# Optimization experiments

Hardware: AMD Instinct MI355X
Metric: run time of the kernel (lower is better)

The kernel has to match this reference:

```python
import jax, jax.numpy as jnp
import numpy as np

DIM = 256      # in_channels == hidden_channels
INNER = 256    # heads * dim_head
HEADS = 4
DH = 64        # dim_head = hidden_channels // num_heads
EDGE_DIM = 512 # 2 * in_channels
FF = 1024      # 4 * dim ff expansion
DEPTH = 2
OUT = 1
N = 50000      # two stacked graphs of 25000 nodes
E = 100000
HALF = 25000


def setup_inputs() -> dict:
    key = jax.random.key(0)
    ks = iter(jax.random.split(key, 32))

    def lin(fan_in, fan_out):
        w = jax.random.normal(next(ks), (DEPTH, fan_in, fan_out), jnp.float32) * (1.0 / np.sqrt(fan_in))
        b = jnp.zeros((DEPTH, fan_out), jnp.float32)
        return w, b

    x = jax.random.normal(next(ks), (N, DIM), jnp.float32)
    edge_index = jax.random.randint(next(ks), (2, E), 0, HALF, dtype=jnp.int32)
    Wq, bq = lin(DIM, INNER)
    Wkv, bkv = lin(DIM, 2 * INNER)
    We, be = lin(EDGE_DIM, INNER)
    Wo, bo = lin(INNER, DIM)
    W1, b1 = lin(DIM, FF)
    W2, b2 = lin(FF, DIM)
    g_attn = jax.random.normal(next(ks), (DEPTH, 3 * DIM, 1), jnp.float32) * (1.0 / np.sqrt(3 * DIM))
    g_ff = jax.random.normal(next(ks), (DEPTH, 3 * DIM, 1), jnp.float32) * (1.0 / np.sqrt(3 * DIM))
    ln1_g = jnp.ones((DEPTH, DIM), jnp.float32); ln1_b = jnp.zeros((DEPTH, DIM), jnp.float32)
    ln2_g = jnp.ones((DEPTH, DIM), jnp.float32); ln2_b = jnp.zeros((DEPTH, DIM), jnp.float32)
    Wout = jax.random.normal(next(ks), (DIM, OUT), jnp.float32) * (1.0 / np.sqrt(DIM))
    bout = jnp.zeros((OUT,), jnp.float32)
    return dict(x=x, edge_index=edge_index, ln1_g=ln1_g, ln1_b=ln1_b, Wq=Wq, bq=bq,
                Wkv=Wkv, bkv=bkv, We=We, be=be, Wo=Wo, bo=bo, g_attn=g_attn,
                ln2_g=ln2_g, ln2_b=ln2_b, W1=W1, b1=b1, W2=W2, b2=b2, g_ff=g_ff,
                Wout=Wout, bout=bout)


def _layer_norm(x, g, b):
    mu = jnp.mean(x, axis=-1, keepdims=True)
    var = jnp.mean(jnp.square(x - mu), axis=-1, keepdims=True)
    return (x - mu) * jax.lax.rsqrt(var + 1e-5) * g + b


def _gated_residual(x, res, w):
    # gate = sigmoid(Linear_no_bias(cat(x, res, x - res)))
    gate = jax.nn.sigmoid(jnp.concatenate([x, res, x - res], axis=-1) @ w)  # [n,1]
    return x * gate + res * (1.0 - gate)


def _forward(x, edge_index, ln1_g, ln1_b, Wq, bq, Wkv, bkv, We, be, Wo, bo, g_attn,
             ln2_g, ln2_b, W1, b1, W2, b2, g_ff, Wout, bout):
    src, dst = edge_index[0], edge_index[1]
    # edge_attr = cat(x[src], x[dst]) as built in DeepGraphTransformer_mse.forward
    edge_attr = jnp.concatenate([x[src], x[dst]], axis=-1)  # [E, 2*DIM]
    nodes = x
    n = nodes.shape[0]
    scale = DH ** -0.5
    for l in range(DEPTH):
        xn = _layer_norm(nodes, ln1_g[l], ln1_b[l])
        q = xn @ Wq[l] + bq[l]                                   # [n, INNER]
        k, v = jnp.split(xn @ Wkv[l] + bkv[l], 2, axis=-1)       # [n, INNER] each
        e = edge_attr @ We[l] + be[l]                            # [E, INNER]
        qe = q[dst].reshape(-1, HEADS, DH)                       # [E,H,Dh]
        ke = (k[src] + e).reshape(-1, HEADS, DH)
        ve = (v[src] + e).reshape(-1, HEADS, DH)
        sim = jnp.einsum('ehd,ehd->eh', qe, ke) * scale          # [E,H]
        smax = jax.ops.segment_max(sim, dst, num_segments=n)     # [n,H] (-inf for empty)
        ez = jnp.exp(sim - smax[dst])
        denom = jax.ops.segment_sum(ez, dst, num_segments=n)
        attn = ez / denom[dst]                                   # softmax over incoming edges
        agg = jax.ops.segment_sum(attn[:, :, None] * ve, dst, num_segments=n)
        attn_out = agg.reshape(n, INNER) @ Wo[l] + bo[l]         # [n, DIM]
        nodes = _gated_residual(attn_out, nodes, g_attn[l])
        xn2 = _layer_norm(nodes, ln2_g[l], ln2_b[l])
        h = jax.nn.gelu(xn2 @ W1[l] + b1[l], approximate=False) @ W2[l] + b2[l]
        nodes = _gated_residual(h, nodes, g_ff[l])
    z = nodes @ Wout + bout                                      # [n, OUT]
    return z


def reference(x, edge_index, ln1_g, ln1_b, Wq, bq, Wkv, bkv, We, be, Wo, bo, g_attn,
              ln2_g, ln2_b, W1, b1, W2, b2, g_ff, Wout, bout):
    z = _forward(x, edge_index, ln1_g, ln1_b, Wq, bq, Wkv, bkv, We, be, Wo, bo, g_attn,
                 ln2_g, ln2_b, W1, b1, W2, b2, g_ff, Wout, bout)
    half = z.shape[0] // 2
    z_old, z_new = z[:half], z[half:]
    return (z_new.reshape(-1), z_old, z_new)
```

## Files before the change

kernel.cpp:

```cpp
#include <hip/hip_runtime.h>
#include <cmath>

#define N_NODES 50000
#define N_EDGES 100000
#define HALF_N  25000
#define DIM     256
#define NDEPTH  2
#define MAXDEG  64

#define WT_QKVE 0
#define WT_WO   393216
#define WT_W1   524288
#define WT_W2   786432
#define WT_LAYER 1048576

typedef __bf16 bf16;
typedef bf16 bf16x8 __attribute__((ext_vector_type(8)));
typedef bf16 bf16x4 __attribute__((ext_vector_type(4)));
typedef float f32x4 __attribute__((ext_vector_type(4)));

__device__ __forceinline__ void lds_barrier() {
  asm volatile("s_waitcnt lgkmcnt(0)" ::: "memory");
  __builtin_amdgcn_s_barrier();
  __builtin_amdgcn_sched_barrier(0);
}

__device__ __forceinline__ float wave_sum(float v) {
  v += __shfl_xor(v, 1);
  v += __shfl_xor(v, 2);
  v += __shfl_xor(v, 4);
  v += __shfl_xor(v, 8);
  v += __shfl_xor(v, 16);
  v += __shfl_xor(v, 32);
  return v;
}

__device__ __forceinline__ float fast_gelu(float v) {
  float ax = fabsf(v) * 0.70710678118654752f;
  float t = __builtin_amdgcn_rcpf(fmaf(0.3275911f, ax, 1.0f));
  float p = t * fmaf(t, fmaf(t, fmaf(t, fmaf(t, 1.061405429f, -1.453152027f),
                                     1.421413741f), -0.284496736f), 0.254829592f);
  float e = __expf(-ax * ax);
  float erfv = fmaf(-p, e, 1.0f);
  float ph = copysignf(erfv, v);
  return 0.5f * v * (1.0f + ph);
}

__global__ void ln0_kernel(const float* __restrict__ in, const float* __restrict__ g,
                           const float* __restrict__ b, bf16* __restrict__ A2) {
  int row = blockIdx.x * 4 + (threadIdx.x >> 6);
  if (row >= HALF_N) return;
  int lane = threadIdx.x & 63;
  float4 x = reinterpret_cast<const float4*>(in + (size_t)row * DIM)[lane];
  float mu = wave_sum(x.x + x.y + x.z + x.w) * (1.0f / DIM);
  float d0 = x.x - mu, d1 = x.y - mu, d2 = x.z - mu, d3 = x.w - mu;
  float var = wave_sum(d0*d0 + d1*d1 + d2*d2 + d3*d3) * (1.0f / DIM);
  float r = rsqrtf(var + 1e-5f);
  float4 gv = reinterpret_cast<const float4*>(g)[lane];
  float4 bv = reinterpret_cast<const float4*>(b)[lane];
  bf16x4 o;
  o[0] = (bf16)(d0 * r * gv.x + bv.x);
  o[1] = (bf16)(d1 * r * gv.y + bv.y);
  o[2] = (bf16)(d2 * r * gv.z + bv.z);
  o[3] = (bf16)(d3 * r * gv.w + bv.w);
  *reinterpret_cast<bf16x4*>(A2 + (size_t)row * 512 + lane * 4) = o;
}

template<int KK, int NJ>
__global__ __launch_bounds__(256, 2) void gemm_nloop(
    const bf16* __restrict__ A, const bf16* __restrict__ Wp,
    const float* __restrict__ bias, bf16* __restrict__ C, int M) {
  constexpr int STEPS = KK / 64;
  __shared__ bf16x8 As[KK * 8];
  __shared__ bf16 Cs[64 * 128];
  const int tid = threadIdx.x;
  const int lane = tid & 63, wv = tid >> 6;
  const int wr = wv >> 1, wc = wv & 1;
  const int lm = lane & 15, kb = (lane >> 4) & 3;
  const int row0 = blockIdx.x * 64;
#pragma unroll
  for (int i = 0; i < KK / 32; ++i) {
    int idx = tid + i * 256;
    int row = idx & 63, k8 = idx >> 6;
    int rga = row0 + row; if (rga >= M) rga = M - 1;
    As[idx] = *reinterpret_cast<const bf16x8*>(A + (size_t)rga * KK + k8 * 8);
  }
  const bf16x8* wb = reinterpret_cast<const bf16x8*>(Wp) + kb * 128 + wc * 64 + lm;
  bf16x8 pfr[4];
#pragma unroll
  for (int ni = 0; ni < 4; ++ni) pfr[ni] = wb[ni * 16];
  lds_barrier();
  for (int jn = 0; jn < NJ; ++jn) {
    f32x4 acc[2][4] = {};
#pragma unroll
    for (int st = 0; st < STEPS; ++st) {
#pragma unroll
      for (int ks = 0; ks < 2; ++ks) {
        bf16x8 bfr[4], af[2];
        if (st == 0 && ks == 0) {
#pragma unroll
          for (int ni = 0; ni < 4; ++ni) bfr[ni] = pfr[ni];
        } else {
#pragma unroll
          for (int ni = 0; ni < 4; ++ni)
            bfr[ni] = wb[(size_t)jn * (KK * 16) + st * 1024 + ks * 512 + ni * 16];
        }
#pragma unroll
        for (int mi = 0; mi < 2; ++mi)
          af[mi] = As[(st * 8 + ks * 4 + kb) * 64 + wr * 32 + mi * 16 + lm];
#pragma unroll
        for (int mi = 0; mi < 2; ++mi)
#pragma unroll
          for (int ni = 0; ni < 4; ++ni)
            acc[mi][ni] = __builtin_amdgcn_mfma_f32_16x16x32_bf16(af[mi], bfr[ni], acc[mi][ni], 0, 0, 0);
      }
    }
    if (jn + 1 < NJ) {
#pragma unroll
      for (int ni = 0; ni < 4; ++ni)
        pfr[ni] = wb[(size_t)(jn + 1) * (KK * 16) + ni * 16];
    }
    lds_barrier();
#pragma unroll
    for (int ni = 0; ni < 4; ++ni) {
      int c = wc * 64 + ni * 16 + lm;
      float bval = bias[jn * 128 + c];
#pragma unroll
      for (int mi = 0; mi < 2; ++mi)
#pragma unroll
        for (int e = 0; e < 4; ++e) {
          int r = wr * 32 + mi * 16 + kb * 4 + e;
          Cs[r * 128 + c] = (bf16)(acc[mi][ni][e] + bval);
        }
    }
    lds_barrier();
    bf16x8* C8 = reinterpret_cast<bf16x8*>(C);
    const bf16x8* Cs8 = (const bf16x8*)Cs;
#pragma unroll
    for (int i = 0; i < 4; ++i) {
      int idx = tid + i * 256;
      int row = idx >> 4, c8 = idx & 15;
      int grow = row0 + row;
      if (grow < M) C8[(size_t)grow * (NJ * 16) + jn * 16 + c8] = Cs8[row * 16 + c8];
    }
  }
}

__global__ __launch_bounds__(256, 2) void wo_fused(
    const bf16* __restrict__ agg, const bf16* __restrict__ A2,
    const bf16* __restrict__ Wp, const float* __restrict__ bvec,
    const float* __restrict__ bo, const int* __restrict__ deg,
    const float* __restrict__ gattn, const float* __restrict__ ln2g,
    const float* __restrict__ ln2b, float* __restrict__ nodes,
    bf16* __restrict__ xn, int rows) {
  __shared__ bf16x8 As[2048];
  __shared__ bf16 Cs[64 * 256];
  const int tid = threadIdx.x;
  const int lane = tid & 63, wv = tid >> 6;
  const int row0 = blockIdx.x * 64;
  if (row0 < HALF_N) {
    const int wr = wv >> 1, wc = wv & 1;
    const int lm = lane & 15, kb = (lane >> 4) & 3;
#pragma unroll
    for (int i = 0; i < 8; ++i) {
      int idx = tid + i * 256;
      int row = idx & 63, k8 = idx >> 6;
      int rga = row0 + row; if (rga >= HALF_N) rga = HALF_N - 1;
      As[idx] = *reinterpret_cast<const bf16x8*>(agg + (size_t)rga * 256 + k8 * 8);
    }
    bf16x8 afx[2][8];
#pragma unroll
    for (int mi = 0; mi < 2; ++mi) {
      int row = row0 + wr * 32 + mi * 16 + lm;
      if (row >= HALF_N) row = HALF_N - 1;
      const bf16* pa = A2 + (size_t)row * 512 + 256 + kb * 8;
#pragma unroll
      for (int t = 0; t < 8; ++t)
        afx[mi][t] = *reinterpret_cast<const bf16x8*>(pa + t * 32);
    }
    lds_barrier();
    const bf16x8* wb = reinterpret_cast<const bf16x8*>(Wp) + kb * 128 + wc * 64 + lm;
    for (int jn = 0; jn < 2; ++jn) {
      f32x4 acc[2][4] = {};
#pragma unroll
      for (int st = 0; st < 8; ++st) {
#pragma unroll
        for (int ks = 0; ks < 2; ++ks) {
          bf16x8 bfr[4], af[2];
#pragma unroll
          for (int ni = 0; ni < 4; ++ni)
            bfr[ni] = wb[jn * 8192 + (st * 8 + ks * 4) * 128 + ni * 16];
#pragma unroll
          for (int mi = 0; mi < 2; ++mi)
            af[mi] = (st < 4) ? As[(st * 8 + ks * 4 + kb) * 64 + wr * 32 + mi * 16 + lm]
                              : afx[mi][(st - 4) * 2 + ks];
#pragma unroll
          for (int mi = 0; mi < 2; ++mi)
#pragma unroll
            for (int ni = 0; ni < 4; ++ni)
              acc[mi][ni] = __builtin_amdgcn_mfma_f32_16x16x32_bf16(af[mi], bfr[ni], acc[mi][ni], 0, 0, 0);
        }
      }
#pragma unroll
      for (int ni = 0; ni < 4; ++ni) {
        int cfull = jn * 128 + wc * 64 + ni * 16 + lm;
        float bval = bvec[cfull];
#pragma unroll
        for (int mi = 0; mi < 2; ++mi)
#pragma unroll
          for (int e = 0; e < 4; ++e) {
            int r = wr * 32 + mi * 16 + kb * 4 + e;
            int ch = (cfull >> 3) ^ (r & 7);
            Cs[r * 256 + ch * 8 + (cfull & 7)] = (bf16)(acc[mi][ni][e] + bval);
          }
      }
    }
    lds_barrier();
    for (int pass = 0; pass < 16; ++pass) {
      int r = pass * 4 + wv;
      int grow = row0 + r;
      float x0, x1, x2, x3;
      if (grow >= HALF_N || deg[grow] == 0) {
        float4 bo4 = reinterpret_cast<const float4*>(bo)[lane];
        x0 = bo4.x; x1 = bo4.y; x2 = bo4.z; x3 = bo4.w;
      } else {
        int ch = (lane >> 1) ^ (r & 7);
        bf16x4 c4 = *reinterpret_cast<const bf16x4*>(Cs + r * 256 + ch * 8 + (lane & 1) * 4);
        x0 = (float)c4[0]; x1 = (float)c4[1]; x2 = (float)c4[2]; x3 = (float)c4[3];
      }
      float4 rv = reinterpret_cast<const float4*>(nodes + (size_t)grow * 256)[lane];
      float4 w0 = reinterpret_cast<const float4*>(gattn)[lane];
      float4 w1 = reinterpret_cast<const float4*>(gattn + 256)[lane];
      float4 w2 = reinterpret_cast<const float4*>(gattn + 512)[lane];
      float dot = x0 * (w0.x + w2.x) + rv.x * (w1.x - w2.x)
                + x1 * (w0.y + w2.y) + rv.y * (w1.y - w2.y)
                + x2 * (w0.z + w2.z) + rv.z * (w1.z - w2.z)
                + x3 * (w0.w + w2.w) + rv.w * (w1.w - w2.w);
      dot = wave_sum(dot);
      float gate = 1.0f / (1.0f + __expf(-dot));
      float n0 = fmaf(x0 - rv.x, gate, rv.x);
      float n1 = fmaf(x1 - rv.y, gate, rv.y);
      float n2 = fmaf(x2 - rv.z, gate, rv.z);
      float n3 = fmaf(x3 - rv.w, gate, rv.w);
      float4 o; o.x = n0; o.y = n1; o.z = n2; o.w = n3;
      reinterpret_cast<float4*>(nodes + (size_t)grow * 256)[lane] = o;
      float mu = wave_sum(n0 + n1 + n2 + n3) * (1.0f / DIM);
      float d0 = n0 - mu, d1 = n1 - mu, d2 = n2 - mu, d3 = n3 - mu;
      float var = wave_sum(d0*d0 + d1*d1 + d2*d2 + d3*d3) * (1.0f / DIM);
      float rs = rsqrtf(var + 1e-5f);
      float4 gv = reinterpret_cast<const float4*>(ln2g)[lane];
      float4 bv = reinterpret_cast<const float4*>(ln2b)[lane];
      bf16x4 ob;
      ob[0] = (bf16)(d0 * rs * gv.x + bv.x);
      ob[1] = (bf16)(d1 * rs * gv.y + bv.y);
      ob[2] = (bf16)(d2 * rs * gv.z + bv.z);
      ob[3] = (bf16)(d3 * rs * gv.w + bv.w);
      *reinterpret_cast<bf16x4*>(xn + (size_t)grow * 256 + lane * 4) = ob;
    }
  } else {
    float4 bo4 = reinterpret_cast<const float4*>(bo)[lane];
    for (int pass = 0; pass < 16; ++pass) {
      int grow = row0 + pass * 4 + wv;
      if (grow >= rows) continue;
      float x0 = bo4.x, x1 = bo4.y, x2 = bo4.z, x3 = bo4.w;
      float4 rv = reinterpret_cast<const float4*>(nodes + (size_t)grow * 256)[lane];
      float4 w0 = reinterpret_cast<const float4*>(gattn)[lane];
      float4 w1 = reinterpret_cast<const float4*>(gattn + 256)[lane];
      float4 w2 = reinterpret_cast<const float4*>(gattn + 512)[lane];
      float dot = x0 * (w0.x + w2.x) + rv.x * (w1.x - w2.x)
                + x1 * (w0.y + w2.y) + rv.y * (w1.y - w2.y)
                + x2 * (w0.z + w2.z) + rv.z * (w1.z - w2.z)
                + x3 * (w0.w + w2.w) + rv.w * (w1.w - w2.w);
      dot = wave_sum(dot);
      float gate = 1.0f / (1.0f + __expf(-dot));
      float n0 = fmaf(x0 - rv.x, gate, rv.x);
      float n1 = fmaf(x1 - rv.y, gate, rv.y);
      float n2 = fmaf(x2 - rv.z, gate, rv.z);
      float n3 = fmaf(x3 - rv.w, gate, rv.w);
      float4 o; o.x = n0; o.y = n1; o.z = n2; o.w = n3;
      reinterpret_cast<float4*>(nodes + (size_t)grow * 256)[lane] = o;
      float mu = wave_sum(n0 + n1 + n2 + n3) * (1.0f / DIM);
      float d0 = n0 - mu, d1 = n1 - mu, d2 = n2 - mu, d3 = n3 - mu;
      float var = wave_sum(d0*d0 + d1*d1 + d2*d2 + d3*d3) * (1.0f / DIM);
      float rs = rsqrtf(var + 1e-5f);
      float4 gv = reinterpret_cast<const float4*>(ln2g)[lane];
      float4 bv = reinterpret_cast<const float4*>(ln2b)[lane];
      bf16x4 ob;
      ob[0] = (bf16)(d0 * rs * gv.x + bv.x);
      ob[1] = (bf16)(d1 * rs * gv.y + bv.y);
      ob[2] = (bf16)(d2 * rs * gv.z + bv.z);
      ob[3] = (bf16)(d3 * rs * gv.w + bv.w);
      *reinterpret_cast<bf16x4*>(xn + (size_t)grow * 256 + lane * 4) = ob;
    }
  }
}

template<int LAST>
__global__ __launch_bounds__(512, 4) void ff_fused(
    const bf16* __restrict__ A, const bf16* __restrict__ W1p,
    const float* __restrict__ b1, const bf16* __restrict__ W2p,
    const float* __restrict__ b2, float* __restrict__ nodes,
    const float* __restrict__ gff, const float* __restrict__ ln1g,
    const float* __restrict__ ln1b, bf16* __restrict__ A2,
    const float* __restrict__ Wout, const float* __restrict__ bout,
    float* __restrict__ out, int M) {
  __shared__ char smem[49152];
  bf16x8* Xs = (bf16x8*)smem;
  bf16*   Cs = (bf16*)smem;
  bf16x8* Hs = (bf16x8*)(smem + 32768);
  const int tid = threadIdx.x;
  const int lane = tid & 63, wv = tid >> 6;
  const int wr = wv >> 2, wc = wv & 3;
  const int lm = lane & 15, kb = (lane >> 4) & 3;
  const int row0 = blockIdx.x * 64;
#pragma unroll
  for (int i = 0; i < 4; ++i) {
    int idx = tid + i * 512;
    int row = idx & 63, k8 = idx >> 6;
    int rga = row0 + row; if (rga >= M) rga = M - 1;
    Xs[idx] = *reinterpret_cast<const bf16x8*>(A + (size_t)rga * 256 + k8 * 8);
  }
  float4 rvf[8];
#pragma unroll
  for (int pass = 0; pass < 8; ++pass) {
    int grow = row0 + pass * 8 + wv;
    if (grow >= M) grow = M - 1;
    rvf[pass] = reinterpret_cast<const float4*>(nodes + (size_t)grow * 256)[lane];
  }
  lds_barrier();
  const bf16x8* w1b = (const bf16x8*)W1p + kb * 128 + wc * 32 + lm;
  const bf16x8* w2b = (const bf16x8*)W2p + kb * 256 + wc * 64 + lm;
  f32x4 acc[2][4] = {};
  bf16* hsb = (bf16*)Hs;
  for (int j = 0; j < 8; ++j) {
    bf16x8 pf2[8];
#pragma unroll
    for (int ks = 0; ks < 2; ++ks)
#pragma unroll
      for (int ni = 0; ni < 4; ++ni)
        pf2[ks * 4 + ni] = w2b[j * 4096 + ks * 1024 + ni * 16];
    f32x4 acc1[2][2] = {};
#pragma unroll
    for (int half = 0; half < 2; ++half) {
#pragma unroll
      for (int ks = 0; ks < 4; ++ks) {
        bf16x8 bfr[2], af[2];
#pragma unroll
        for (int ni = 0; ni < 2; ++ni)
          bfr[ni] = w1b[j * 4096 + half * 2048 + ks * 512 + ni * 16];
#pragma unroll
        for (int mi = 0; mi < 2; ++mi)
          af[mi] = Xs[(half * 16 + ks * 4 + kb) * 64 + wr * 32 + mi * 16 + lm];
#pragma unroll
        for (int mi = 0; mi < 2; ++mi)
#pragma unroll
          for (int ni = 0; ni < 2; ++ni)
            acc1[mi][ni] = __builtin_amdgcn_mfma_f32_16x16x32_bf16(af[mi], bfr[ni], acc1[mi][ni], 0, 0, 0);
      }
    }
    lds_barrier();
#pragma unroll
    for (int ni = 0; ni < 2; ++ni) {
      int c = wc * 32 + ni * 16 + lm;
      float bval = b1[j * 128 + c];
#pragma unroll
      for (int mi = 0; mi < 2; ++mi)
#pragma unroll
        for (int e = 0; e < 4; ++e) {
          int r = wr * 32 + mi * 16 + kb * 4 + e;
          float v = fast_gelu(acc1[mi][ni][e] + bval);
          hsb[((c >> 3) * 64 + r) * 8 + (c & 7)] = (bf16)v;
        }
    }
    lds_barrier();
#pragma unroll
    for (int h2 = 0; h2 < 2; ++h2) {
#pragma unroll
      for (int ks = 0; ks < 2; ++ks) {
        bf16x8 bfr[4], af[2];
#pragma unroll
        for (int ni = 0; ni < 4; ++ni)
          bfr[ni] = (h2 == 0) ? pf2[ks * 4 + ni]
                              : w2b[j * 4096 + 2048 + ks * 1024 + ni * 16];
#pragma unroll
        for (int mi = 0; mi < 2; ++mi)
          af[mi] = Hs[(h2 * 8 + ks * 4 + kb) * 64 + wr * 32 + mi * 16 + lm];
#pragma unroll
        for (int mi = 0; mi < 2; ++mi)
#pragma unroll
          for (int ni = 0; ni < 4; ++ni)
            acc[mi][ni] = __builtin_amdgcn_mfma_f32_16x16x32_bf16(af[mi], bfr[ni], acc[mi][ni], 0, 0, 0);
      }
    }
  }
#pragma unroll
  for (int ni = 0; ni < 4; ++ni) {
    int c = wc * 64 + ni * 16 + lm;
    float bval = b2[c];
#pragma unroll
    for (int mi = 0; mi < 2; ++mi)
#pragma unroll
      for (int e = 0; e < 4; ++e) {
        int r = wr * 32 + mi * 16 + kb * 4 + e;
        int ch = (c >> 3) ^ (r & 7);
        Cs[r * 256 + ch * 8 + (c & 7)] = (bf16)(acc[mi][ni][e] + bval);
      }
  }
  lds_barrier();
  for (int pass = 0; pass < 8; ++pass) {
    int r = pass * 8 + wv;
    int grow = row0 + r;
    if (grow >= M) continue;
    int ch = (lane >> 1) ^ (r & 7);
    bf16x4 c4 = *reinterpret_cast<const bf16x4*>(Cs + r * 256 + ch * 8 + (lane & 1) * 4);
    float x0 = (float)c4[0], x1 = (float)c4[1], x2 = (float)c4[2], x3 = (float)c4[3];
    float4 rv = rvf[pass];
    float4 w0 = reinterpret_cast<const float4*>(gff)[lane];
    float4 w1 = reinterpret_cast<const float4*>(gff + 256)[lane];
    float4 w2 = reinterpret_cast<const float4*>(gff + 512)[lane];
    float dot = x0 * (w0.x + w2.x) + rv.x * (w1.x - w2.x)
              + x1 * (w0.y + w2.y) + rv.y * (w1.y - w2.y)
              + x2 * (w0.z + w2.z) + rv.z * (w1.z - w2.z)
              + x3 * (w0.w + w2.w) + rv.w * (w1.w - w2.w);
    dot = wave_sum(dot);
    float gate = 1.0f / (1.0f + __expf(-dot));
    float n0 = fmaf(x0 - rv.x, gate, rv.x);
    float n1 = fmaf(x1 - rv.y, gate, rv.y);
    float n2 = fmaf(x2 - rv.z, gate, rv.z);
    float n3 = fmaf(x3 - rv.w, gate, rv.w);
    if (LAST) {
      float4 wo4 = reinterpret_cast<const float4*>(Wout)[lane];
      float z = n0 * wo4.x + n1 * wo4.y + n2 * wo4.z + n3 * wo4.w;
      z = wave_sum(z);
      if (lane == 0) {
        z += bout[0];
        if (grow < HALF_N) {
          out[HALF_N + grow] = z;
        } else {
          int jj = grow - HALF_N;
          out[jj] = z;
          out[2 * HALF_N + jj] = z;
        }
      }
    } else {
      float4 o; o.x = n0; o.y = n1; o.z = n2; o.w = n3;
      reinterpret_cast<float4*>(nodes + (size_t)grow * 256)[lane] = o;
      if (grow < HALF_N) {
        float mu = wave_sum(n0 + n1 + n2 + n3) * (1.0f / DIM);
        float d0 = n0 - mu, d1 = n1 - mu, d2 = n2 - mu, d3 = n3 - mu;
        float var = wave_sum(d0*d0 + d1*d1 + d2*d2 + d3*d3) * (1.0f / DIM);
        float rs = rsqrtf(var + 1e-5f);
        float4 gv = reinterpret_cast<const float4*>(ln1g)[lane];
        float4 bv = reinterpret_cast<const float4*>(ln1b)[lane];
        bf16x4 ob;
        ob[0] = (bf16)(d0 * rs * gv.x + bv.x);
        ob[1] = (bf16)(d1 * rs * gv.y + bv.y);
        ob[2] = (bf16)(d2 * rs * gv.z + bv.z);
        ob[3] = (bf16)(d3 * rs * gv.w + bv.w);
        *reinterpret_cast<bf16x4*>(A2 + (size_t)grow * 512 + lane * 4) = ob;
      }
    }
  }
}

__global__ void ell_build(const int* __restrict__ ei, int* __restrict__ deg,
                          int* __restrict__ ell) {
  int e = blockIdx.x * 256 + threadIdx.x;
  if (e >= N_EDGES) return;
  int s = ei[e], d = ei[N_EDGES + e];
  int pos = atomicAdd(&deg[d], 1);
  if (pos < MAXDEG) ell[d * MAXDEG + pos] = s;
}

__global__ void attn_gather(const int* __restrict__ deg, const int* __restrict__ ell,
                            const bf16* __restrict__ qkv, bf16* __restrict__ agg) {
  int d = blockIdx.x * 4 + (threadIdx.x >> 6);
  if (d >= HALF_N) return;
  int lane = threadIdx.x & 63;
  int cnt = deg[d]; if (cnt > MAXDEG) cnt = MAXDEG;
  const bf16* qr = qkv + (size_t)d * 768;
  bf16x4 qb = *reinterpret_cast<const bf16x4*>(qr + lane * 4);
  float q0 = (float)qb[0], q1 = (float)qb[1], q2 = (float)qb[2], q3 = (float)qb[3];
  float m = -INFINITY, den = 0.0f, a0 = 0.0f, a1 = 0.0f, a2 = 0.0f, a3 = 0.0f;
  int i = 0;
  for (; i + 2 <= cnt; i += 2) {
    int s0 = ell[d * MAXDEG + i];
    int s1 = ell[d * MAXDEG + i + 1];
    bf16x8 k0 = *reinterpret_cast<const bf16x8*>(qkv + (size_t)s0 * 768 + 256 + lane * 8);
    bf16x8 k1 = *reinterpret_cast<const bf16x8*>(qkv + (size_t)s1 * 768 + 256 + lane * 8);
    float p0 = q0 * (float)k0[0] + q1 * (float)k0[1] + q2 * (float)k0[2] + q3 * (float)k0[3];
    float p1 = q0 * (float)k1[0] + q1 * (float)k1[1] + q2 * (float)k1[2] + q3 * (float)k1[3];
    p0 += __shfl_xor(p0, 1); p1 += __shfl_xor(p1, 1);
    p0 += __shfl_xor(p0, 2); p1 += __shfl_xor(p1, 2);
    p0 += __shfl_xor(p0, 4); p1 += __shfl_xor(p1, 4);
    p0 += __shfl_xor(p0, 8); p1 += __shfl_xor(p1, 8);
    float s0v = p0 * 0.125f, s1v = p1 * 0.125f;
    float nm = fmaxf(m, fmaxf(s0v, s1v));
    float sc = __expf(m - nm);
    float w0 = __expf(s0v - nm), w1 = __expf(s1v - nm);
    den = den * sc + w0 + w1;
    a0 = a0 * sc + w0 * (float)k0[4] + w1 * (float)k1[4];
    a1 = a1 * sc + w0 * (float)k0[5] + w1 * (float)k1[5];
    a2 = a2 * sc + w0 * (float)k0[6] + w1 * (float)k1[6];
    a3 = a3 * sc + w0 * (float)k0[7] + w1 * (float)k1[7];
    m = nm;
  }
  if (i < cnt) {
    int s = ell[d * MAXDEG + i];
    bf16x8 kv8 = *reinterpret_cast<const bf16x8*>(qkv + (size_t)s * 768 + 256 + lane * 8);
    float p = q0 * (float)kv8[0] + q1 * (float)kv8[1] + q2 * (float)kv8[2] + q3 * (float)kv8[3];
    p += __shfl_xor(p, 1); p += __shfl_xor(p, 2);
    p += __shfl_xor(p, 4); p += __shfl_xor(p, 8);
    float sim = p * 0.125f;
    float nm = fmaxf(m, sim);
    float sc = __expf(m - nm);
    float w = __expf(sim - nm);
    den = den * sc + w;
    a0 = a0 * sc + w * (float)kv8[4];
    a1 = a1 * sc + w * (float)kv8[5];
    a2 = a2 * sc + w * (float)kv8[6];
    a3 = a3 * sc + w * (float)kv8[7];
    m = nm;
  }
  bf16x4 o;
  if (cnt > 0) {
    float inv = 1.0f / den;
    o[0] = (bf16)(a0 * inv);
    o[1] = (bf16)(a1 * inv);
    o[2] = (bf16)(a2 * inv);
    o[3] = (bf16)(a3 * inv);
  } else {
    o[0] = (bf16)0.0f; o[1] = (bf16)0.0f; o[2] = (bf16)0.0f; o[3] = (bf16)0.0f;
  }
  *reinterpret_cast<bf16x4*>(agg + (size_t)d * DIM + lane * 4) = o;
}

__global__ void prep_w(const float* __restrict__ Wq, const float* __restrict__ Wkv,
                       const float* __restrict__ We, const float* __restrict__ Wo,
                       const float* __restrict__ W1, const float* __restrict__ W2,
                       bf16* __restrict__ wt) {
  int idx = blockIdx.x * 256 + threadIdx.x;
  if (idx >= 2 * WT_LAYER) return;
  int l = idx / WT_LAYER, r = idx % WT_LAYER;
  float v;
  if (r < 393216) {
    int jn = r >> 16, t = r & 65535;
    int k8 = t >> 10, u = t & 1023, n = u >> 3, e = u & 7;
    int ncol = jn * 128 + n, k = k8 * 8 + e;
    if (ncol < 256) {
      v = (k < 256) ? Wq[l * 65536 + k * 256 + ncol] : 0.0f;
    } else {
      int u2 = ncol - 256;
      int c = (u2 >> 3) * 4 + (u2 & 3);
      int half = (u2 >> 2) & 1;
      if (k < 256) v = Wkv[l * 131072 + k * 512 + half * 256 + c];
      else         v = We[l * 131072 + (k - 256) * 256 + c];
    }
  } else if (r < 524288) {
    int rr = r - 393216;
    int jn = rr >> 16, t = rr & 65535;
    int k8 = t >> 10, u = t & 1023, n = u >> 3, e = u & 7;
    int k = k8 * 8 + e;
    if (k >= 256) return;
    v = Wo[l * 65536 + k * 256 + jn * 128 + n];
  } else if (r < 786432) {
    int rr = r - 524288;
    int j = rr >> 15, t = rr & 32767;
    int k8 = t >> 10, u = t & 1023, n = u >> 3, e = u & 7;
    v = W1[l * 262144 + (k8 * 8 + e) * 1024 + j * 128 + n];
  } else {
    int rr = r - 786432;
    int j = rr >> 15, t = rr & 32767;
    int k8 = t >> 11, u = t & 2047, n = u >> 3, e = u & 7;
    v = W2[l * 262144 + (j * 128 + k8 * 8 + e) * 256 + n];
  }
  wt[idx] = (bf16)v;
}

__global__ void prep_weff(const float* __restrict__ We, const float* __restrict__ Wo,
                          bf16* __restrict__ wt) {
  int idx = blockIdx.x * 256 + threadIdx.x;
  if (idx >= 2 * 65536) return;
  int l = idx >> 16, r = idx & 65535;
  int k = r >> 8, n = r & 255;
  const float* wer = We + l * 131072 + (256 + k) * 256;
  const float* wor = Wo + l * 65536 + n;
  float acc = 0.0f;
#pragma unroll 4
  for (int m = 0; m < 256; ++m) acc += wer[m] * wor[m * 256];
  int kf = 256 + k;
  size_t off = (size_t)l * WT_LAYER + WT_WO +
               (n >> 7) * 65536 + (kf >> 3) * 1024 + (n & 127) * 8 + (kf & 7);
  wt[off] = (bf16)acc;
}

__global__ void prep_bvec(const float* __restrict__ be, const float* __restrict__ Wo,
                          const float* __restrict__ bo, float* __restrict__ biasq) {
  int idx = blockIdx.x * 256 + threadIdx.x;
  if (idx >= 512) return;
  int l = idx >> 8, n = idx & 255;
  const float* ber = be + l * 256;
  const float* wor = Wo + l * 65536 + n;
  float acc = bo[l * 256 + n];
#pragma unroll 4
  for (int m = 0; m < 256; ++m) acc += ber[m] * wor[m * 256];
  biasq[1536 + l * 256 + n] = acc;
}

__global__ void prep_bias(const float* __restrict__ bq, const float* __restrict__ bkv,
                          float* __restrict__ biasq) {
  int i = blockIdx.x * 256 + threadIdx.x;
  if (i >= 1536) return;
  int l = i / 768, n = i % 768;
  float v;
  if (n < 256) v = bq[l * 256 + n];
  else {
    int u2 = n - 256;
    int c = (u2 >> 3) * 4 + (u2 & 3);
    int half = (u2 >> 2) & 1;
    v = bkv[l * 512 + half * 256 + c];
  }
  biasq[i] = v;
}

__global__ void prep_x(const float* __restrict__ x, bf16* __restrict__ A2) {
  int i = blockIdx.x * 256 + threadIdx.x;
  if (i >= HALF_N * 64) return;
  int row = i >> 6, c = i & 63;
  float4 v = reinterpret_cast<const float4*>(x)[i];
  bf16x4 o;
  o[0] = (bf16)v.x; o[1] = (bf16)v.y; o[2] = (bf16)v.z; o[3] = (bf16)v.w;
  *reinterpret_cast<bf16x4*>(A2 + (size_t)row * 512 + 256 + c * 4) = o;
}

extern "C" void kernel_launch(void* const* d_in, const int* in_sizes, int n_in,
                              void* d_out, int out_size, void* d_ws, size_t ws_size,
                              hipStream_t stream) {
  const float* x     = (const float*)d_in[0];
  const int*   ei    = (const int*)d_in[1];
  const float* ln1_g = (const float*)d_in[2];
  const float* ln1_b = (const float*)d_in[3];
  const float* Wq    = (const float*)d_in[4];
  const float* bq    = (const float*)d_in[5];
  const float* Wkv   = (const float*)d_in[6];
  const float* bkv   = (const float*)d_in[7];
  const float* We    = (const float*)d_in[8];
  const float* be    = (const float*)d_in[9];
  const float* Wo    = (const float*)d_in[10];
  const float* bo    = (const float*)d_in[11];
  const float* g_attn= (const float*)d_in[12];
  const float* ln2_g = (const float*)d_in[13];
  const float* ln2_b = (const float*)d_in[14];
  const float* W1    = (const float*)d_in[15];
  const float* b1    = (const float*)d_in[16];
  const float* W2    = (const float*)d_in[17];
  const float* b2    = (const float*)d_in[18];
  const float* g_ff  = (const float*)d_in[19];
  const float* Wout  = (const float*)d_in[20];
  const float* bout  = (const float*)d_in[21];
  float* out = (float*)d_out;

  char* base = (char*)d_ws;
  float* nodes   = (float*)base;  base += (size_t)N_NODES * DIM * 4;
  bf16*  A2      = (bf16*)base;   base += (size_t)HALF_N * 512 * 2;
  bf16*  xn_bf   = (bf16*)base;   base += (size_t)N_NODES * DIM * 2;
  bf16*  qkv     = (bf16*)base;   base += (size_t)HALF_N * 768 * 2;
  bf16*  agg     = (bf16*)base;   base += (size_t)HALF_N * DIM * 2;
  bf16*  wt      = (bf16*)base;   base += (size_t)2 * WT_LAYER * 2;
  float* biasq   = (float*)base;  base += 2048 * 4;
  int*   deg     = (int*)base;    base += HALF_N * 4;
  int*   ell     = (int*)base;    base += (size_t)HALF_N * MAXDEG * 4;

  hipMemcpyAsync(nodes, x, (size_t)N_NODES * DIM * sizeof(float),
                 hipMemcpyDeviceToDevice, stream);
  prep_w<<<(2 * WT_LAYER + 255) / 256, 256, 0, stream>>>(Wq, Wkv, We, Wo, W1, W2, wt);
  prep_weff<<<(2 * 65536 + 255) / 256, 256, 0, stream>>>(We, Wo, wt);
  prep_bvec<<<2, 256, 0, stream>>>(be, Wo, bo, biasq);
  prep_bias<<<6, 256, 0, stream>>>(bq, bkv, biasq);
  prep_x<<<(HALF_N * 64 + 255) / 256, 256, 0, stream>>>(x, A2);
  hipMemsetAsync(deg, 0, HALF_N * sizeof(int), stream);
  ell_build<<<(N_EDGES + 255) / 256, 256, 0, stream>>>(ei, deg, ell);

  const int GP_H = (HALF_N + 63) / 64;
  const int GP_N = (N_NODES + 63) / 64;

  for (int l = 0; l < NDEPTH; ++l) {
    const bf16* wl = wt + (size_t)l * WT_LAYER;
    if (l == 0)
      ln0_kernel<<<(HALF_N + 3) / 4, 256, 0, stream>>>(x, ln1_g, ln1_b, A2);
    gemm_nloop<512, 6><<<GP_H, 256, 0, stream>>>(A2, wl + WT_QKVE, biasq + l * 768, qkv, HALF_N);
    attn_gather<<<(HALF_N + 3) / 4, 256, 0, stream>>>(deg, ell, qkv, agg);
    wo_fused<<<GP_N, 256, 0, stream>>>(agg, A2, wl + WT_WO, biasq + 1536 + l * 256,
                                       bo + l * DIM, deg, g_attn + l * 768,
                                       ln2_g + l * DIM, ln2_b + l * DIM,
                                       nodes, xn_bf, N_NODES);
    if (l < NDEPTH - 1) {
      ff_fused<0><<<GP_N, 512, 0, stream>>>(
          xn_bf, wl + WT_W1, b1 + l * 1024, wl + WT_W2, b2 + l * DIM,
          nodes, g_ff + l * 768, ln1_g + (l + 1) * DIM, ln1_b + (l + 1) * DIM, A2,
          nullptr, nullptr, nullptr, N_NODES);
    } else {
      ff_fused<1><<<GP_N, 512, 0, stream>>>(
          xn_bf, wl + WT_W1, b1 + l * 1024, wl + WT_W2, b2 + l * DIM,
          nodes, g_ff + l * 768, nullptr, nullptr, nullptr,
          Wout, bout, out, N_NODES);
    }
  }
}
```

Measured before the change: 568.1 us.

## Remap GEMM warps to full-row column slices and double-buffer FF hidden tile

Both gemm_nloop and ff_fused now give each wave all 64 rows and a narrower column slice, instead of a 2D row/column split. Each wave loads fewer weight fragments from global memory but more A fragments from LDS. ff_fused also double-buffers the GELU hidden tile in LDS, which removes one barrier per j iteration but raises shared memory to 64KB. The residual node rows are now loaded at the epilogue rather than held in registers across the loop, lowering register pressure at the cost of exposed load latency.

Result: faster. 499.7 us (-12.0%).

```diff
diff --git a/kernel.cpp b/kernel.cpp
--- a/kernel.cpp
+++ b/kernel.cpp
@@ -75,7 +75,6 @@
   __shared__ bf16 Cs[64 * 128];
   const int tid = threadIdx.x;
   const int lane = tid & 63, wv = tid >> 6;
-  const int wr = wv >> 1, wc = wv & 1;
   const int lm = lane & 15, kb = (lane >> 4) & 3;
   const int row0 = blockIdx.x * 64;
 #pragma unroll
@@ -85,51 +84,50 @@
     int rga = row0 + row; if (rga >= M) rga = M - 1;
     As[idx] = *reinterpret_cast<const bf16x8*>(A + (size_t)rga * KK + k8 * 8);
   }
-  const bf16x8* wb = reinterpret_cast<const bf16x8*>(Wp) + kb * 128 + wc * 64 + lm;
-  bf16x8 pfr[4];
-#pragma unroll
-  for (int ni = 0; ni < 4; ++ni) pfr[ni] = wb[ni * 16];
+  const bf16x8* wb = reinterpret_cast<const bf16x8*>(Wp) + kb * 128 + wv * 32 + lm;
+  bf16x8 pfr[2];
+#pragma unroll
+  for (int ni = 0; ni < 2; ++ni) pfr[ni] = wb[ni * 16];
   lds_barrier();
   for (int jn = 0; jn < NJ; ++jn) {
-    f32x4 acc[2][4] = {};
+    f32x4 acc[4][2] = {};
 #pragma unroll
     for (int st = 0; st < STEPS; ++st) {
 #pragma unroll
       for (int ks = 0; ks < 2; ++ks) {
-        bf16x8 bfr[4], af[2];
+        bf16x8 bfr[2], af[4];
         if (st == 0 && ks == 0) {
-#pragma unroll
-          for (int ni = 0; ni < 4; ++ni) bfr[ni] = pfr[ni];
+          bfr[0] = pfr[0]; bfr[1] = pfr[1];
         } else {
 #pragma unroll
-          for (int ni = 0; ni < 4; ++ni)
+          for (int ni = 0; ni < 2; ++ni)
             bfr[ni] = wb[(size_t)jn * (KK * 16) + st * 1024 + ks * 512 + ni * 16];
         }
 #pragma unroll
-        for (int mi = 0; mi < 2; ++mi)
-          af[mi] = As[(st * 8 + ks * 4 + kb) * 64 + wr * 32 + mi * 16 + lm];
-#pragma unroll
-        for (int mi = 0; mi < 2; ++mi)
-#pragma unroll
-          for (int ni = 0; ni < 4; ++ni)
+        for (int mi = 0; mi < 4; ++mi)
+          af[mi] = As[(st * 8 + ks * 4 + kb) * 64 + mi * 16 + lm];
+#pragma unroll
+        for (int mi = 0; mi < 4; ++mi)
+#pragma unroll
+          for (int ni = 0; ni < 2; ++ni)
             acc[mi][ni] = __builtin_amdgcn_mfma_f32_16x16x32_bf16(af[mi], bfr[ni], acc[mi][ni], 0, 0, 0);
       }
     }
     if (jn + 1 < NJ) {
 #pragma unroll
-      for (int ni = 0; ni < 4; ++ni)
+      for (int ni = 0; ni < 2; ++ni)
         pfr[ni] = wb[(size_t)(jn + 1) * (KK * 16) + ni * 16];
     }
     lds_barrier();
 #pragma unroll
-    for (int ni = 0; ni < 4; ++ni) {
-      int c = wc * 64 + ni * 16 + lm;
+    for (int ni = 0; ni < 2; ++ni) {
+      int c = wv * 32 + ni * 16 + lm;
       float bval = bias[jn * 128 + c];
 #pragma unroll
-      for (int mi = 0; mi < 2; ++mi)
+      for (int mi = 0; mi < 4; ++mi)
 #pragma unroll
         for (int e = 0; e < 4; ++e) {
-          int r = wr * 32 + mi * 16 + kb * 4 + e;
+          int r = mi * 16 + kb * 4 + e;
           Cs[r * 128 + c] = (bf16)(acc[mi][ni][e] + bval);
         }
     }
@@ -304,13 +302,12 @@
     const float* __restrict__ ln1b, bf16* __restrict__ A2,
     const float* __restrict__ Wout, const float* __restrict__ bout,
     float* __restrict__ out, int M) {
-  __shared__ char smem[49152];
+  __shared__ char smem[65536];
   bf16x8* Xs = (bf16x8*)smem;
   bf16*   Cs = (bf16*)smem;
   bf16x8* Hs = (bf16x8*)(smem + 32768);
   const int tid = threadIdx.x;
   const int lane = tid & 63, wv = tid >> 6;
-  const int wr = wv >> 2, wc = wv & 3;
   const int lm = lane & 15, kb = (lane >> 4) & 3;
   const int row0 = blockIdx.x * 64;
 #pragma unroll
@@ -320,88 +317,76 @@
     int rga = row0 + row; if (rga >= M) rga = M - 1;
     Xs[idx] = *reinterpret_cast<const bf16x8*>(A + (size_t)rga * 256 + k8 * 8);
   }
-  float4 rvf[8];
-#pragma unroll
-  for (int pass = 0; pass < 8; ++pass) {
-    int grow = row0 + pass * 8 + wv;
-    if (grow >= M) grow = M - 1;
-    rvf[pass] = reinterpret_cast<const float4*>(nodes + (size_t)grow * 256)[lane];
-  }
   lds_barrier();
-  const bf16x8* w1b = (const bf16x8*)W1p + kb * 128 + wc * 32 + lm;
-  const bf16x8* w2b = (const bf16x8*)W2p + kb * 256 + wc * 64 + lm;
-  f32x4 acc[2][4] = {};
-  bf16* hsb = (bf16*)Hs;
+  const bf16x8* w1b = (const bf16x8*)W1p + kb * 128 + wv * 16 + lm;
+  const bf16x8* w2b = (const bf16x8*)W2p + kb * 256 + wv * 32 + lm;
+  f32x4 acc[4][2] = {};
   for (int j = 0; j < 8; ++j) {
-    bf16x8 pf2[8];
+    bf16x8 pf2[4];
 #pragma unroll
     for (int ks = 0; ks < 2; ++ks)
 #pragma unroll
-      for (int ni = 0; ni < 4; ++ni)
-        pf2[ks * 4 + ni] = w2b[j * 4096 + ks * 1024 + ni * 16];
-    f32x4 acc1[2][2] = {};
+      for (int ni = 0; ni < 2; ++ni)
+        pf2[ks * 2 + ni] = w2b[j * 4096 + ks * 1024 + ni * 16];
+    f32x4 acc1[4] = {};
 #pragma unroll
     for (int half = 0; half < 2; ++half) {
 #pragma unroll
       for (int ks = 0; ks < 4; ++ks) {
-        bf16x8 bfr[2], af[2];
-#pragma unroll
-        for (int ni = 0; ni < 2; ++ni)
-          bfr[ni] = w1b[j * 4096 + half * 2048 + ks * 512 + ni * 16];
-#pragma unroll
-        for (int mi = 0; mi < 2; ++mi)
-          af[mi] = Xs[(half * 16 + ks * 4 + kb) * 64 + wr * 32 + mi * 16 + lm];
-#pragma unroll
-        for (int mi = 0; mi < 2; ++mi)
-#pragma unroll
-          for (int ni = 0; ni < 2; ++ni)
-            acc1[mi][ni] = __builtin_amdgcn_mfma_f32_16x16x32_bf16(af[mi], bfr[ni], acc1[mi][ni], 0, 0, 0);
-      }
-    }
-    lds_barrier();
-#pragma unroll
-    for (int ni = 0; ni < 2; ++ni) {
-      int c = wc * 32 + ni * 16 + lm;
+        bf16x8 bfr = w1b[j * 4096 + half * 2048 + ks * 512];
+        bf16x8 af[4];
+#pragma unroll
+        for (int mi = 0; mi < 4; ++mi)
+          af[mi] = Xs[(half * 16 + ks * 4 + kb) * 64 + mi * 16 + lm];
+#pragma unroll
+        for (int mi = 0; mi < 4; ++mi)
+          acc1[mi] = __builtin_amdgcn_mfma_f32_16x16x32_bf16(af[mi], bfr, acc1[mi], 0, 0, 0);
+      }
+    }
+    {
+      bf16* hsb = (bf16*)(Hs + (j & 1) * 1024);
+      int c = wv * 16 + lm;
       float bval = b1[j * 128 + c];
 #pragma unroll
-      for (int mi = 0; mi < 2; ++mi)
+      for (int mi = 0; mi < 4; ++mi)
 #pragma unroll
         for (int e = 0; e < 4; ++e) {
-          int r = wr * 32 + mi * 16 + kb * 4 + e;
-          float v = fast_gelu(acc1[mi][ni][e] + bval);
+          int r = mi * 16 + kb * 4 + e;
+          float v = fast_gelu(acc1[mi][e] + bval);
           hsb[((c >> 3) * 64 + r) * 8 + (c & 7)] = (bf16)v;
         }
     }
     lds_barrier();
+    const bf16x8* hb = Hs + (j & 1) * 1024;
 #pragma unroll
     for (int h2 = 0; h2 < 2; ++h2) {
 #pragma unroll
       for (int ks = 0; ks < 2; ++ks) {
-        bf16x8 bfr[4], af[2];
-#pragma unroll
-        for (int ni = 0; ni < 4; ++ni)
-          bfr[ni] = (h2 == 0) ? pf2[ks * 4 + ni]
+        bf16x8 bfr[2], af[4];
+#pragma unroll
+        for (int ni = 0; ni < 2; ++ni)
+          bfr[ni] = (h2 == 0) ? pf2[ks * 2 + ni]
                               : w2b[j * 4096 + 2048 + ks * 1024 + ni * 16];
 #pragma unroll
-        for (int mi = 0; mi < 2; ++mi)
-          af[mi] = Hs[(h2 * 8 + ks * 4 + kb) * 64 + wr * 32 + mi * 16 + lm];
-#pragma unroll
-        for (int mi = 0; mi < 2; ++mi)
-#pragma unroll
-          for (int ni = 0; ni < 4; ++ni)
+        for (int mi = 0; mi < 4; ++mi)
+          af[mi] = hb[(h2 * 8 + ks * 4 + kb) * 64 + mi * 16 + lm];
+#pragma unroll
+        for (int mi = 0; mi < 4; ++mi)
+#pragma unroll
+          for (int ni = 0; ni < 2; ++ni)
             acc[mi][ni] = __builtin_amdgcn_mfma_f32_16x16x32_bf16(af[mi], bfr[ni], acc[mi][ni], 0, 0, 0);
       }
     }
   }
 #pragma unroll
-  for (int ni = 0; ni < 4; ++ni) {
-    int c = wc * 64 + ni * 16 + lm;
+  for (int ni = 0; ni < 2; ++ni) {
+    int c = wv * 32 + ni * 16 + lm;
     float bval = b2[c];
 #pragma unroll
-    for (int mi = 0; mi < 2; ++mi)
+    for (int mi = 0; mi < 4; ++mi)
 #pragma unroll
       for (int e = 0; e < 4; ++e) {
-        int r = wr * 32 + mi * 16 + kb * 4 + e;
+        int r = mi * 16 + kb * 4 + e;
         int ch = (c >> 3) ^ (r & 7);
         Cs[r * 256 + ch * 8 + (c & 7)] = (bf16)(acc[mi][ni][e] + bval);
       }
@@ -414,7 +399,7 @@
     int ch = (lane >> 1) ^ (r & 7);
     bf16x4 c4 = *reinterpret_cast<const bf16x4*>(Cs + r * 256 + ch * 8 + (lane & 1) * 4);
     float x0 = (float)c4[0], x1 = (float)c4[1], x2 = (float)c4[2], x3 = (float)c4[3];
-    float4 rv = rvf[pass];
+    float4 rv = reinterpret_cast<const float4*>(nodes + (size_t)grow * 256)[lane];
     float4 w0 = reinterpret_cast<const float4*>(gff)[lane];
     float4 w1 = reinterpret_cast<const float4*>(gff + 256)[lane];
     float4 w2 = reinterpret_cast<const float4*>(gff + 512)[lane];
```
